# Optimization experiments

Hardware: AMD Instinct MI355X
Metric: run time of the kernel (lower is better)

Reference implementation:

```python
import jax, jax.numpy as jnp
import numpy as np

EPS = 1e-5


def _conv3x3(x, w, b):
    # x: [B,Cin,H,W], w: [Cout,Cin,3,3]
    y = jax.lax.conv_general_dilated(x, w, (1, 1), 'SAME',
                                     dimension_numbers=('NCHW', 'OIHW', 'NCHW'))
    return y + b[None, :, None, None]


def _gn_per_channel(x, w, b):
    # GroupNorm with num_groups == num_channels: per-channel spatial normalization
    mu = x.mean(axis=(2, 3), keepdims=True)
    var = x.var(axis=(2, 3), keepdims=True)
    return (x - mu) * jax.lax.rsqrt(var + EPS) * w[None, :, None, None] + b[None, :, None, None]


def _p1x1(x, w, b):
    # 1x1 conv as channel matmul. w: [Cout,Cin]
    return jnp.einsum('oc,bchw->bohw', w, x) + b[None, :, None, None]


def _cell(x, h, c, m, lc, conv_w, conv_b, gn1_w, gn1_b, convL_w, convL_b, gn2_w, gn2_b,
          wq, bq, wk, bk, wk2, bk2, wv, bv, wv2, bv2, wz, bz, wm, bm):
    # --- first conv-gate block ---
    cc = _gn_per_channel(_conv3x3(jnp.concatenate([x, h], axis=1), conv_w, conv_b), gn1_w, gn1_b)
    ci, cf, co, cg = jnp.split(cc, 4, axis=1)
    c_next = jax.nn.sigmoid(cf) * c + jax.nn.sigmoid(ci) * jnp.tanh(cg)
    # --- second (long) conv-gate block ---
    ccl = _gn_per_channel(_conv3x3(jnp.concatenate([h, c_next], axis=1), convL_w, convL_b), gn2_w, gn2_b)
    li, lf, lo, lg = jnp.split(ccl, 4, axis=1)
    lc_next = jax.nn.sigmoid(lf) * lc + jax.nn.sigmoid(li) * jnp.tanh(lg)
    c_next = jax.nn.sigmoid(lo) * jnp.tanh(lc_next)
    h_mid = jax.nn.sigmoid(co) * jnp.tanh(c_next)
    # --- SAM spatial self-attention memory ---
    B, C, H, W = h_mid.shape
    HW = H * W
    Kh = _p1x1(h_mid, wk, bk).reshape(B, -1, HW)          # [B,A,HW]
    Qh = _p1x1(h_mid, wq, bq).reshape(B, -1, HW).transpose(0, 2, 1)  # [B,HW,A]
    Vh = _p1x1(h_mid, wv, bv).reshape(B, C, HW)           # [B,C,HW]
    Km = _p1x1(m, wk2, bk2).reshape(B, -1, HW)
    Vm = _p1x1(m, wv2, bv2).reshape(B, C, HW)
    Ah = jax.nn.softmax(jnp.einsum('bpa,baq->bpq', Qh, Kh), axis=-1)  # [B,HW,HW]
    Zh = jnp.einsum('bpq,bcq->bcp', Ah, Vh).reshape(B, C, H, W)
    Am = jax.nn.softmax(jnp.einsum('bpa,baq->bpq', Qh, Km), axis=-1)
    Zm = jnp.einsum('bpq,bcq->bcp', Am, Vm).reshape(B, C, H, W)
    Z = _p1x1(jnp.concatenate([Zh, Zm], axis=1), wz, bz)  # [B,2C,H,W]
    comb = _p1x1(jnp.concatenate([Z, h_mid], axis=1), wm, bm)  # [B,3C,H,W]
    mo, mg, mi = jnp.split(comb, 3, axis=1)
    mi = jax.nn.sigmoid(mi)
    m_next = (1.0 - mi) * m + mi * jnp.tanh(mg)
    h_next = jax.nn.sigmoid(mo) * m_next
    return h_next, c_next, m_next, lc_next


def setup_inputs() -> dict:
    key = jax.random.key(0)
    B, Cin, Ch, A, H, W = 16, 64, 64, 32, 32, 32
    ks = jax.random.split(key, 24)
    s = 0.05
    inp = {
        'x': jax.random.normal(ks[0], (B, Cin, H, W), jnp.float32),
        'h': jax.random.normal(ks[1], (B, Ch, H, W), jnp.float32),
        'c': jax.random.normal(ks[2], (B, Ch, H, W), jnp.float32),
        'm': jax.random.normal(ks[3], (B, Ch, H, W), jnp.float32),
        'lc': jax.random.normal(ks[4], (B, Ch, H, W), jnp.float32),
        'conv_w': jax.random.normal(ks[5], (4 * Ch, Cin + Ch, 3, 3), jnp.float32) * s,
        'conv_b': jnp.zeros((4 * Ch,), jnp.float32),
        'gn1_w': jnp.ones((4 * Ch,), jnp.float32),
        'gn1_b': jnp.zeros((4 * Ch,), jnp.float32),
        'convL_w': jax.random.normal(ks[6], (4 * Ch, 2 * Ch, 3, 3), jnp.float32) * s,
        'convL_b': jnp.zeros((4 * Ch,), jnp.float32),
        'gn2_w': jnp.ones((4 * Ch,), jnp.float32),
        'gn2_b': jnp.zeros((4 * Ch,), jnp.float32),
        'wq': jax.random.normal(ks[7], (A, Ch), jnp.float32) * s,
        'bq': jnp.zeros((A,), jnp.float32),
        'wk': jax.random.normal(ks[8], (A, Ch), jnp.float32) * s,
        'bk': jnp.zeros((A,), jnp.float32),
        'wk2': jax.random.normal(ks[9], (A, Ch), jnp.float32) * s,
        'bk2': jnp.zeros((A,), jnp.float32),
        'wv': jax.random.normal(ks[10], (Ch, Ch), jnp.float32) * s,
        'bv': jnp.zeros((Ch,), jnp.float32),
        'wv2': jax.random.normal(ks[11], (Ch, Ch), jnp.float32) * s,
        'bv2': jnp.zeros((Ch,), jnp.float32),
        'wz': jax.random.normal(ks[12], (2 * Ch, 2 * Ch), jnp.float32) * s,
        'bz': jnp.zeros((2 * Ch,), jnp.float32),
        'wm': jax.random.normal(ks[13], (3 * Ch, 3 * Ch), jnp.float32) * s,
        'bm': jnp.zeros((3 * Ch,), jnp.float32),
    }
    return inp


def reference(x, h, c, m, lc, conv_w, conv_b, gn1_w, gn1_b, convL_w, convL_b, gn2_w, gn2_b,
              wq, bq, wk, bk, wk2, bk2, wv, bv, wv2, bv2, wz, bz, wm, bm):
    return _cell(x, h, c, m, lc, conv_w, conv_b, gn1_w, gn1_b, convL_w, convL_b, gn2_w, gn2_b,
                 wq, bq, wk, bk, wk2, bk2, wv, bv, wv2, bv2, wz, bz, wm, bm)
```

## Files before the change

kernel.cpp:

```cpp
#include <hip/hip_runtime.h>

#define DEV __device__ __forceinline__

typedef __attribute__((ext_vector_type(8))) __bf16 bf16x8;
typedef __attribute__((ext_vector_type(4))) float f32x4;
typedef __attribute__((ext_vector_type(8))) unsigned short ushort8;
typedef __attribute__((ext_vector_type(2))) unsigned short ushort2v;
typedef __attribute__((ext_vector_type(2))) unsigned int uint2v;

DEV float sigmoidf_(float x){ return 1.0f/(1.0f + __expf(-x)); }
DEV float tanhf_(float x){
    x = fminf(15.0f, fmaxf(-15.0f, x));
    float e = __expf(2.0f*x);
    return (e - 1.0f)/(e + 1.0f);
}
DEV unsigned short f2bf(float f){
    unsigned u = __builtin_bit_cast(unsigned, f);
    unsigned r = (u + 0x7FFFu + ((u>>16)&1u)) >> 16;
    return (unsigned short)r;
}
DEV float bf2f(unsigned short u){
    return __builtin_bit_cast(float, ((unsigned)u)<<16);
}
DEV unsigned cvt_pk_bf16(float lo, float hi){
    unsigned r;
    asm("v_cvt_pk_bf16_f32 %0, %1, %2" : "=v"(r) : "v"(lo), "v"(hi));
    return r;
}

__global__ __launch_bounds__(256)
void prep_kernel(const float* __restrict__ conv_w, const float* __restrict__ convL_w,
                 const float* __restrict__ wz, const float* __restrict__ wm,
                 const float* __restrict__ wq, const float* __restrict__ wk,
                 const float* __restrict__ wv, const float* __restrict__ wk2,
                 const float* __restrict__ wv2,
                 const float* __restrict__ x, const float* __restrict__ h,
                 unsigned short* __restrict__ wpk1, unsigned short* __restrict__ wpk2,
                 unsigned short* __restrict__ wzb, unsigned short* __restrict__ wmb,
                 unsigned short* __restrict__ wph, unsigned short* __restrict__ wpm,
                 unsigned short* __restrict__ buf1, unsigned short* __restrict__ buf2)
{
    __shared__ float tile[128][65];
    if (blockIdx.x < 1152) {
        int oidx = blockIdx.x*256 + threadIdx.x;
        {
            int ci5 = oidx & 31;
            int co  = (oidx >> 5) & 255;
            int kch = oidx >> 13;
            int cic = kch / 9, tap = kch - 9*cic;
            int src = co*1152 + (cic*32 + ci5)*9 + tap;
            wpk1[oidx] = f2bf(conv_w[src]);
            wpk2[oidx] = f2bf(convL_w[src]);
        }
        if (oidx < 128*128) wzb[oidx] = f2bf(wz[oidx]);
        if (oidx < 192*192) wmb[oidx] = f2bf(wm[oidx]);
        if (oidx < 32*64){
            wph[oidx]        = f2bf(wq[oidx]);
            wph[2048 + oidx] = f2bf(wk[oidx]);
            wpm[oidx]        = f2bf(wk2[oidx]);
        }
        if (oidx < 64*64){
            wph[4096 + oidx] = f2bf(wv[oidx]);
            wpm[2048 + oidx] = f2bf(wv2[oidx]);
        }
    } else if (blockIdx.x < 1184) {
        int bx2 = blockIdx.x - 1152;
        int b = bx2 >> 1;
        unsigned short* buf = (bx2 & 1) ? buf2 : buf1;
        for (int i = threadIdx.x; i < 8448; i += 256){
            int px = i >> 6, u = i & 63;
            int rr, cc2;
            if (px < 34)      { rr = 0;         cc2 = px; }
            else if (px < 68) { rr = 33;        cc2 = px-34; }
            else if (px < 100){ rr = px-68+1;   cc2 = 0; }
            else              { rr = px-100+1;  cc2 = 33; }
            reinterpret_cast<unsigned*>(buf + (size_t)(b*1156 + rr*34 + cc2)*128)[u] = 0u;
        }
    } else {
        int i  = blockIdx.x - 1184;
        int b  = (i&7)*2 + ((i>>3)&1);
        int p0 = (i>>4) * 64;
        int t  = threadIdx.x;
        for (int k=t;k<8192;k+=256){
            int ci = k>>6, pp = k&63;
            const float* s = (ci<64) ? x + (size_t)(b*64+ci)*1024
                                     : h + (size_t)(b*64+ci-64)*1024;
            tile[ci][pp] = s[p0+pp];
        }
        __syncthreads();
        for (int k=t;k<4096;k+=256){
            int pp = k>>6, c2 = k&63;
            int p  = p0 + pp;
            size_t pidx = (size_t)(b*1156 + ((p>>5)+1)*34 + (p&31) + 1);
            ushort2v v;
            v.x = f2bf(tile[c2*2][pp]);
            v.y = f2bf(tile[c2*2+1][pp]);
            *reinterpret_cast<ushort2v*>(buf1 + pidx*128 + c2*2) = v;
            if (c2 >= 32)
                *reinterpret_cast<ushort2v*>(buf2 + pidx*128 + (c2-32)*2) = v;
        }
    }
}

__global__ __launch_bounds__(256, 2)
void conv_mfma_kernel(const unsigned short* __restrict__ inp,
                      const unsigned short* __restrict__ wpk,
                      const float* __restrict__ bias,
                      unsigned short* __restrict__ out,
                      float* __restrict__ statsS, float* __restrict__ statsQ)
{
    const int bid = blockIdx.x;
    const int b   = (bid&7)*2 + ((bid>>3)&1);
    const int co0 = ((bid>>4)&3) * 64;
    const int rt  = bid>>6;
    const int r0  = rt * 4;
    const int t   = threadIdx.x;
    const int l   = t & 63;
    const int wv  = t >> 6;
    const int l15 = l & 15;
    const int lhi = l >> 4;

    __shared__ __align__(16) unsigned short in_t[26112];

    {
        const char* gsrc = reinterpret_cast<const char*>(inp + (size_t)(b*1156 + r0*34)*128);
#pragma unroll
        for (int it = 0; it < 13; ++it){
            unsigned lbase = (unsigned)(it*4096 + wv*1024);
            if (lbase < 52224u){
                unsigned beta = lbase + (unsigned)l*16u;
                unsigned soff = (beta & ~255u) + ((beta & 0xF0u) ^ (((beta>>8)&7u)<<4));
                __builtin_amdgcn_global_load_lds(
                    (const __attribute__((address_space(1))) void*)(gsrc + soff),
                    (__attribute__((address_space(3))) void*)(
                        (__attribute__((address_space(3))) char*)in_t + lbase),
                    16, 0, 0);
            }
        }
    }

    f32x4 acc[4][2];
#pragma unroll
    for (int i=0;i<4;i++)
#pragma unroll
        for (int f=0;f<2;f++)
            acc[i][f] = (f32x4){0.f,0.f,0.f,0.f};

    bf16x8 areg[4][4], breg[3][2];
#define LDA_(K, SLOT) do { const unsigned short* wrow_ = wpk + ((K)*256 + co0)*32; \
        for (int i_=0;i_<4;i_++) areg[SLOT][i_] = *reinterpret_cast<const bf16x8*>(wrow_ + (i_*16 + l15)*32 + lhi*8); } while(0)
#define LDB_(K, SLOT) do { const int cic_ = (K)/9, tap_ = (K) - 9*((K)/9); \
        const int ky_ = tap_/3, kx_ = tap_ - 3*(tap_/3); \
        for (int f_=0;f_<2;f_++){ int pl_ = (wv + ky_)*34 + (f_*16 + l15 + kx_); \
            unsigned by_ = (unsigned)(pl_*256 + cic_*64 + lhi*16) ^ (((unsigned)pl_ & 7u) << 4); \
            breg[SLOT][f_] = *reinterpret_cast<const bf16x8*>(reinterpret_cast<const char*>(in_t) + by_); } } while(0)

    LDA_(0, 0); LDA_(1, 1); LDA_(2, 2);
    __syncthreads();
    LDB_(0, 0); LDB_(1, 1);
#pragma unroll
    for (int k=0; k<36; ++k){
        const int as = k & 3, bs = k % 3;
        if (k+3 < 36) LDA_(k+3, (k+3)&3);
        if (k+2 < 36) LDB_(k+2, (k+2)%3);
        __builtin_amdgcn_s_setprio(1);
#pragma unroll
        for (int i=0;i<4;i++){
            acc[i][0] = __builtin_amdgcn_mfma_f32_16x16x32_bf16(areg[as][i], breg[bs][0], acc[i][0], 0,0,0);
            acc[i][1] = __builtin_amdgcn_mfma_f32_16x16x32_bf16(areg[as][i], breg[bs][1], acc[i][1], 0,0,0);
        }
        __builtin_amdgcn_s_setprio(0);
    }
#undef LDA_
#undef LDB_

    __syncthreads();
    float* red = reinterpret_cast<float*>(in_t);

    const int orow = r0 + wv;
    float s_ir[4][4], q_ir[4][4];
#pragma unroll
    for (int i=0;i<4;i++){
        int cobase = co0 + i*16 + lhi*4;
#pragma unroll
        for (int r=0;r<4;r++){
            float bs = bias[cobase+r];
            float e0 = acc[i][0][r] + bs;
            float e1 = acc[i][1][r] + bs;
            out[(size_t)(b*256 + cobase + r)*1024 + orow*32 + l15]      = f2bf(e0);
            out[(size_t)(b*256 + cobase + r)*1024 + orow*32 + 16 + l15] = f2bf(e1);
            s_ir[i][r] = e0 + e1;
            q_ir[i][r] = e0*e0 + e1*e1;
        }
    }
#pragma unroll
    for (int i=0;i<4;i++)
#pragma unroll
        for (int r=0;r<4;r++){
            float s = s_ir[i][r], q = q_ir[i][r];
            s += __shfl_xor(s,1); q += __shfl_xor(q,1);
            s += __shfl_xor(s,2); q += __shfl_xor(q,2);
            s += __shfl_xor(s,4); q += __shfl_xor(q,4);
            s += __shfl_xor(s,8); q += __shfl_xor(q,8);
            s_ir[i][r] = s; q_ir[i][r] = q;
        }
    if (l15 == 0){
#pragma unroll
        for (int i=0;i<4;i++)
#pragma unroll
            for (int r=0;r<4;r++){
                red[wv*64 + i*16 + lhi*4 + r]       = s_ir[i][r];
                red[256 + wv*64 + i*16 + lhi*4 + r] = q_ir[i][r];
            }
    }
    __syncthreads();
    if (t < 64){
        float S = red[t]+red[64+t]+red[128+t]+red[192+t];
        float Q = red[256+t]+red[320+t]+red[384+t]+red[448+t];
        statsS[((size_t)b*8 + rt)*256 + co0 + t] = S;
        statsQ[((size_t)b*8 + rt)*256 + co0 + t] = Q;
    }
}

__global__ __launch_bounds__(256)
void gn_gate1_kernel(const unsigned short* __restrict__ cc,
                     const float* __restrict__ statsS, const float* __restrict__ statsQ,
                     const float* __restrict__ gnw, const float* __restrict__ gnb,
                     const float* __restrict__ c_in,
                     unsigned short* __restrict__ buf2, unsigned short* __restrict__ sig_pm)
{
    const int bid = blockIdx.x;
    const int b   = (bid&7)*2 + ((bid>>3)&1);
    const int p0  = (bid>>4) * 32;
    const int t  = threadIdx.x;
    __shared__ float sc[256][2];
    __shared__ __align__(16) unsigned short cct[10240];

    {
        float S=0.f, Q=0.f;
#pragma unroll
        for (int part=0; part<8; ++part){
            S += statsS[((size_t)b*8 + part)*256 + t];
            Q += statsQ[((size_t)b*8 + part)*256 + t];
        }
        float mu  = S*(1.0f/1024.0f);
        float var = Q*(1.0f/1024.0f) - mu*mu;
        float rs  = rsqrtf(var + 1e-5f);
        float gw  = gnw[t];
        sc[t][0] = rs*gw;
        sc[t][1] = gnb[t] - mu*rs*gw;
    }
    for (int it=t; it<1024; it+=256){
        int row = it>>2, oct = it&3;
        ushort8 v = *reinterpret_cast<const ushort8*>(
            cc + (size_t)(b*256+row)*1024 + p0 + oct*8);
        *reinterpret_cast<ushort8*>(cct + row*40 + oct*8) = v;
    }
    __syncthreads();

    const int p = t & 31, cg = t >> 5;
    float cn[8], so[8];
#pragma unroll
    for (int j=0;j<8;j++){
        int ch = cg*8 + j;
        float xg[4];
#pragma unroll
        for (int g=0; g<4; g++){
            int row = g*64 + ch;
            float v = bf2f(cct[row*40 + p]);
            xg[g] = v*sc[row][0] + sc[row][1];
        }
        float cv = c_in[(size_t)(b*64+ch)*1024 + p0 + p];
        cn[j] = sigmoidf_(xg[1])*cv + sigmoidf_(xg[0])*tanhf_(xg[3]);
        so[j] = sigmoidf_(xg[2]);
    }
    ushort8 v0, s0;
#pragma unroll
    for (int j=0;j<8;j++){ v0[j]=f2bf(cn[j]); s0[j]=f2bf(so[j]); }
    int pg = p0 + p;
    size_t pidx = (size_t)(b*1156 + ((pg>>5)+1)*34 + (pg&31) + 1);
    *reinterpret_cast<ushort8*>(buf2 + pidx*128 + 64 + cg*8) = v0;
    *reinterpret_cast<ushort8*>(sig_pm + (size_t)(b*1024 + pg)*64 + cg*8) = s0;
}

__global__ __launch_bounds__(256)
void gn2_proj_kernel(const unsigned short* __restrict__ cc,
                     const float* __restrict__ statsS, const float* __restrict__ statsQ,
                     const float* __restrict__ gnw, const float* __restrict__ gnb,
                     const float* __restrict__ lc_in, const unsigned short* __restrict__ sig_pm,
                     const float* __restrict__ m_in,
                     const unsigned short* __restrict__ wph, const unsigned short* __restrict__ wpm,
                     const float* __restrict__ bq, const float* __restrict__ bk,
                     const float* __restrict__ bv, const float* __restrict__ bk2,
                     const float* __restrict__ bv2,
                     float* __restrict__ out_lc, float* __restrict__ out_c,
                     unsigned short* __restrict__ hT,
                     unsigned short* __restrict__ Qb, unsigned short* __restrict__ Khb,
                     unsigned short* __restrict__ Kmb,
                     unsigned short* __restrict__ Vhb, unsigned short* __restrict__ Vmb)
{
    const int bid = blockIdx.x;
    const int b   = (bid&7)*2 + ((bid>>3)&1);
    const int p0  = (bid>>4) * 32;
    const int t  = threadIdx.x;
    const int l  = t & 63;
    const int w  = t >> 6;
    const int l15 = l & 15, lhi = l >> 4;

    __shared__ float sc[256][2];
    __shared__ __align__(16) unsigned short cct[10240];

    {
        float S=0.f, Q=0.f;
#pragma unroll
        for (int part=0; part<8; ++part){
            S += statsS[((size_t)b*8 + part)*256 + t];
            Q += statsQ[((size_t)b*8 + part)*256 + t];
        }
        float mu  = S*(1.0f/1024.0f);
        float var = Q*(1.0f/1024.0f) - mu*mu;
        float rs  = rsqrtf(var + 1e-5f);
        float gw  = gnw[t];
        sc[t][0] = rs*gw;
        sc[t][1] = gnb[t] - mu*rs*gw;
    }
    for (int it=t; it<1024; it+=256){
        int row = it>>2, oct = it&3;
        ushort8 v = *reinterpret_cast<const ushort8*>(
            cc + (size_t)(b*256+row)*1024 + p0 + oct*8);
        *reinterpret_cast<ushort8*>(cct + row*40 + oct*8) = v;
    }
    __syncthreads();

    const int p = t & 31, cg = t >> 5;
    const size_t prow = (size_t)(b*1024 + p0 + p);
    float hm[8], mr[8];
    {
        ushort8 sv = *reinterpret_cast<const ushort8*>(sig_pm + prow*64 + cg*8);
#pragma unroll
        for (int j=0;j<8;j++){
            int ch = cg*8 + j;
            float xg[4];
#pragma unroll
            for (int g=0; g<4; g++){
                int row = g*64 + ch;
                float v = bf2f(cct[row*40 + p]);
                xg[g] = v*sc[row][0] + sc[row][1];
            }
            float lv  = lc_in[(size_t)(b*64+ch)*1024 + p0 + p];
            float lcn = sigmoidf_(xg[1])*lv + sigmoidf_(xg[0])*tanhf_(xg[3]);
            float cnx = sigmoidf_(xg[2])*tanhf_(lcn);
            out_lc[(size_t)(b*64+ch)*1024 + p0 + p] = lcn;
            out_c [(size_t)(b*64+ch)*1024 + p0 + p] = cnx;
            hm[j] = bf2f(sv[j])*tanhf_(cnx);
            mr[j] = m_in[(size_t)(b*64+ch)*1024 + p0 + p];
        }
    }
    __syncthreads();

    {
        ushort8 h0, m0;
#pragma unroll
        for (int j=0;j<8;j++){ h0[j]=f2bf(hm[j]); m0[j]=f2bf(mr[j]); }
        unsigned hb = (unsigned)(p*128) + (((unsigned)(cg*16)) ^ ((unsigned)(p&7)<<4));
        *reinterpret_cast<ushort8*>(reinterpret_cast<char*>(cct) + hb) = h0;
        *reinterpret_cast<ushort8*>(reinterpret_cast<char*>(cct) + 4096 + hb) = m0;
        *reinterpret_cast<ushort8*>(hT + prow*64 + cg*8) = h0;
    }
    __syncthreads();

    const int pass = w >> 1;
    const int pix  = (w&1)*16 + l15;
    const unsigned xsw = ((unsigned)(pix&7)) << 4;
    if (pass == 0){
        f32x4 dh[8];
#pragma unroll
        for (int i=0;i<8;i++) dh[i] = (f32x4){0.f,0.f,0.f,0.f};
#pragma unroll
        for (int ks=0; ks<2; ++ks){
            unsigned xb = (unsigned)(pix*128) + (((unsigned)(ks*64 + lhi*16)) ^ xsw);
            bf16x8 xh = *reinterpret_cast<const bf16x8*>(reinterpret_cast<const char*>(cct) + xb);
            __builtin_amdgcn_s_setprio(1);
#pragma unroll
            for (int ocf=0; ocf<8; ocf++){
                bf16x8 af = *reinterpret_cast<const bf16x8*>(
                    wph + (size_t)(ocf*16 + l15)*64 + ks*32 + lhi*8);
                dh[ocf] = __builtin_amdgcn_mfma_f32_16x16x32_bf16(af, xh, dh[ocf], 0,0,0);
            }
            __builtin_amdgcn_s_setprio(0);
        }
#pragma unroll
        for (int ocf=0; ocf<4; ocf++)
#pragma unroll
            for (int r=0;r<4;r++){
                int vc = ocf*16 + lhi*4 + r;
                Vhb[(size_t)(b*64+vc)*1024 + p0 + pix] = f2bf(dh[4+ocf][r] + bv[vc]);
            }
#pragma unroll
        for (int ocf=0; ocf<2; ocf++)
#pragma unroll
            for (int r=0;r<4;r++){
                int qc = ocf*16 + lhi*4 + r;
                unsigned byq = (unsigned)(pix*128) + (((unsigned)(qc*2))      ^ xsw);
                unsigned byk = (unsigned)(pix*128) + (((unsigned)(64 + qc*2)) ^ xsw);
                *reinterpret_cast<unsigned short*>(reinterpret_cast<char*>(cct) + 8192 + byq)
                    = f2bf(dh[ocf][r]   + bq[qc]);
                *reinterpret_cast<unsigned short*>(reinterpret_cast<char*>(cct) + 8192 + byk)
                    = f2bf(dh[2+ocf][r] + bk[qc]);
            }
    } else {
        f32x4 dm[6];
#pragma unroll
        for (int i=0;i<6;i++) dm[i] = (f32x4){0.f,0.f,0.f,0.f};
#pragma unroll
        for (int ks=0; ks<2; ++ks){
            unsigned xb = (unsigned)(pix*128) + (((unsigned)(ks*64 + lhi*16)) ^ xsw);
            bf16x8 xm = *reinterpret_cast<const bf16x8*>(
                reinterpret_cast<const char*>(cct) + 4096 + xb);
            __builtin_amdgcn_s_setprio(1);
#pragma unroll
            for (int ocf=0; ocf<6; ocf++){
                bf16x8 am = *reinterpret_cast<const bf16x8*>(
                    wpm + (size_t)(ocf*16 + l15)*64 + ks*32 + lhi*8);
                dm[ocf] = __builtin_amdgcn_mfma_f32_16x16x32_bf16(am, xm, dm[ocf], 0,0,0);
            }
            __builtin_amdgcn_s_setprio(0);
        }
#pragma unroll
        for (int ocf=0; ocf<4; ocf++)
#pragma unroll
            for (int r=0;r<4;r++){
                int vc = ocf*16 + lhi*4 + r;
                Vmb[(size_t)(b*64+vc)*1024 + p0 + pix] = f2bf(dm[2+ocf][r] + bv2[vc]);
            }
#pragma unroll
        for (int ocf=0; ocf<2; ocf++)
#pragma unroll
            for (int r=0;r<4;r++){
                int qc = ocf*16 + lhi*4 + r;
                unsigned byq = (unsigned)(pix*128) + (((unsigned)(qc*2)) ^ xsw);
                *reinterpret_cast<unsigned short*>(reinterpret_cast<char*>(cct) + 12288 + byq)
                    = f2bf(dm[ocf][r] + bk2[qc]);
            }
    }
    __syncthreads();

    {
        int pr = t>>3, oct = t&7;
        unsigned byte = (unsigned)(pr*128) + (((unsigned)(oct*16)) ^ ((unsigned)(pr&7)<<4));
        ushort8 v = *reinterpret_cast<const ushort8*>(
            reinterpret_cast<const char*>(cct) + 8192 + byte);
        if (oct < 4) *reinterpret_cast<ushort8*>(Qb  + (size_t)(b*1024+p0+pr)*32 + oct*8) = v;
        else         *reinterpret_cast<ushort8*>(Khb + (size_t)(b*1024+p0+pr)*32 + (oct-4)*8) = v;
    }
    if (t < 128){
        int pr = t>>2, oct = t&3;
        unsigned byte = (unsigned)(pr*128) + (((unsigned)(oct*16)) ^ ((unsigned)(pr&7)<<4));
        ushort8 v = *reinterpret_cast<const ushort8*>(
            reinterpret_cast<const char*>(cct) + 12288 + byte);
        *reinterpret_cast<ushort8*>(Kmb + (size_t)(b*1024+p0+pr)*32 + oct*8) = v;
    }
}

__global__ __launch_bounds__(256)
void attn_final_kernel(const unsigned short* __restrict__ Qb,
                       const unsigned short* __restrict__ Kh,
                       const unsigned short* __restrict__ Km,
                       const unsigned short* __restrict__ Vh,
                       const unsigned short* __restrict__ Vm,
                       const unsigned short* __restrict__ hT,
                       const unsigned short* __restrict__ wzb,
                       const unsigned short* __restrict__ wmb,
                       const float* __restrict__ bz, const float* __restrict__ bm,
                       const float* __restrict__ m_in,
                       float* __restrict__ out_h, float* __restrict__ out_m)
{
    const int bid  = blockIdx.x;
    const int xcd  = bid & 7;
    const int slot = bid >> 3;
    const int b    = xcd*2 + (slot>>5);
    const int p0   = (slot & 31) * 32;
    const int t   = threadIdx.x;
    const int l   = t & 63;
    const int w   = t >> 6;
    const int l15 = l & 15, g = l >> 4;
    const int pass = w >> 1;
    const int ph   = w & 1;

    __shared__ __align__(16) unsigned short Kt[2][2][2560];
    __shared__ __align__(16) unsigned short Vt[2][2][4096];
    __shared__ __align__(16) unsigned short Pt[2][2048];
    __shared__ __align__(16) unsigned short Bs[32*192];

    const bf16x8 qa = *reinterpret_cast<const bf16x8*>(
        Qb + (size_t)(b*1024 + p0 + ph*16 + l15)*32 + g*8);

    const int hrow = t>>3, hoct = t&7;
    const ushort8 hreg = *reinterpret_cast<const ushort8*>(
        hT + (size_t)(b*1024 + p0 + hrow)*64 + hoct*8);

    float m_run = -1e30f, l_run = 0.0f;
    f32x4 acc[4];
#pragma unroll
    for (int cf=0;cf<4;cf++) acc[cf] = (f32x4){0.f,0.f,0.f,0.f};

    const int krow = t>>2, koct = t&3;
    const int vrow = t>>3, voct = t&7;
    const unsigned kwb  = (unsigned)(krow*80 + koct*16);
    const unsigned vwb0 = (unsigned)(vrow*128)      + (((unsigned)voct*16) ^ ((unsigned)(vrow&7)<<4));
    const unsigned vwb1 = (unsigned)((vrow+32)*128) + (((unsigned)voct*16) ^ ((unsigned)((vrow+32)&7)<<4));

    ushort8 kr0, kr1, vv0, vv1, vv2, vv3;
#define LDSTAGE(Q0N) do { \
        kr0 = *reinterpret_cast<const ushort8*>(Kh + (size_t)(b*1024 + (Q0N) + krow)*32 + koct*8); \
        kr1 = *reinterpret_cast<const ushort8*>(Km + (size_t)(b*1024 + (Q0N) + krow)*32 + koct*8); \
        vv0 = *reinterpret_cast<const ushort8*>(Vh + (size_t)(b*64 + vrow)*1024 + (Q0N) + voct*8); \
        vv1 = *reinterpret_cast<const ushort8*>(Vh + (size_t)(b*64 + vrow+32)*1024 + (Q0N) + voct*8); \
        vv2 = *reinterpret_cast<const ushort8*>(Vm + (size_t)(b*64 + vrow)*1024 + (Q0N) + voct*8); \
        vv3 = *reinterpret_cast<const ushort8*>(Vm + (size_t)(b*64 + vrow+32)*1024 + (Q0N) + voct*8); \
    } while(0)
#define WRSTAGE(BUF) do { \
        *reinterpret_cast<ushort8*>(reinterpret_cast<char*>(Kt[0][BUF]) + kwb)  = kr0; \
        *reinterpret_cast<ushort8*>(reinterpret_cast<char*>(Kt[1][BUF]) + kwb)  = kr1; \
        *reinterpret_cast<ushort8*>(reinterpret_cast<char*>(Vt[0][BUF]) + vwb0) = vv0; \
        *reinterpret_cast<ushort8*>(reinterpret_cast<char*>(Vt[0][BUF]) + vwb1) = vv1; \
        *reinterpret_cast<ushort8*>(reinterpret_cast<char*>(Vt[1][BUF]) + vwb0) = vv2; \
        *reinterpret_cast<ushort8*>(reinterpret_cast<char*>(Vt[1][BUF]) + vwb1) = vv3; \
    } while(0)

    LDSTAGE(0);
    WRSTAGE(0);
    __syncthreads();

    const unsigned prow = (unsigned)(ph*16 + l15);
    const unsigned psw  = (prow & 7u) << 4;
    char* Pbase = reinterpret_cast<char*>(Pt[pass]);

    for (int it=0; it<16; ++it){
        const int cur = it & 1;
        if (it < 15) LDSTAGE((it+1)*64);

        f32x4 s2[4];
        __builtin_amdgcn_s_setprio(1);
#pragma unroll
        for (int qt=0; qt<4; qt++){
            const bf16x8 kb = *reinterpret_cast<const bf16x8*>(
                reinterpret_cast<const char*>(Kt[pass][cur]) + (qt*16 + l15)*80 + g*16);
            s2[qt] = __builtin_amdgcn_mfma_f32_16x16x32_bf16(kb, qa, (f32x4){0.f,0.f,0.f,0.f}, 0,0,0);
        }
        __builtin_amdgcn_s_setprio(0);

        float pm = s2[0][0];
#pragma unroll
        for (int qt=0; qt<4; qt++)
#pragma unroll
            for (int r=0;r<4;r++) pm = fmaxf(pm, s2[qt][r]);
        pm = fmaxf(pm, __shfl_xor(pm, 16));
        pm = fmaxf(pm, __shfl_xor(pm, 32));

        if (!__all(pm <= m_run + 8.0f)){
            float mn = fmaxf(m_run, pm);
            float f  = __expf(m_run - mn);
            m_run = mn;
            l_run *= f;
#pragma unroll
            for (int r=0;r<4;r++){
                float fr = __shfl(f, (l & 48) | ((l>>4)*4 + r), 64);
#pragma unroll
                for (int cf=0;cf<4;cf++) acc[cf][r] *= fr;
            }
        }

        float e[4][4];
        float lsum = 0.f;
#pragma unroll
        for (int qt=0; qt<4; qt++)
#pragma unroll
            for (int r=0;r<4;r++){
                float ev = __expf(s2[qt][r] - m_run);
                e[qt][r] = ev;
                lsum += ev;
            }
        lsum += __shfl_xor(lsum, 16);
        lsum += __shfl_xor(lsum, 32);
        l_run += lsum;

#pragma unroll
        for (int qt=0; qt<4; qt++){
            uint2v pk;
            pk.x = cvt_pk_bf16(e[qt][0], e[qt][1]);
            pk.y = cvt_pk_bf16(e[qt][2], e[qt][3]);
            unsigned byte = prow*128 + (((unsigned)(qt*32 + g*8)) ^ psw);
            *reinterpret_cast<uint2v*>(Pbase + byte) = pk;
        }

        __builtin_amdgcn_s_setprio(1);
#pragma unroll
        for (int ks=0;ks<2;ks++){
            unsigned abyte = prow*128 + (((unsigned)(ks*64 + g*16)) ^ psw);
            const bf16x8 pa = *reinterpret_cast<const bf16x8*>(Pbase + abyte);
#pragma unroll
            for (int cf=0;cf<4;cf++){
                unsigned vrw = (unsigned)(cf*16 + l15);
                unsigned vbyte = vrw*128 + (((unsigned)(ks*64 + g*16)) ^ ((vrw&7u)<<4));
                const bf16x8 vb = *reinterpret_cast<const bf16x8*>(
                    reinterpret_cast<const char*>(Vt[pass][cur]) + vbyte);
                acc[cf] = __builtin_amdgcn_mfma_f32_16x16x32_bf16(pa, vb, acc[cf], 0,0,0);
            }
        }
        __builtin_amdgcn_s_setprio(0);

        if (it < 15) WRSTAGE(cur^1);
        __syncthreads();
    }
#undef LDSTAGE
#undef WRSTAGE

    {
        float rl = 1.0f / l_run;
        float rr[4];
#pragma unroll
        for (int r=0;r<4;r++) rr[r] = __shfl(rl, (l & 48) | ((l>>4)*4 + r), 64);
#pragma unroll
        for (int cf=0;cf<4;cf++)
#pragma unroll
            for (int r=0;r<4;r++){
                unsigned pix = (unsigned)(ph*16 + g*4 + r);
                unsigned cch = (unsigned)(pass*64 + cf*16 + l15);
                unsigned byte = pix*384 + ((cch*2) ^ ((pix&7u)<<4));
                *reinterpret_cast<unsigned short*>(reinterpret_cast<char*>(Bs) + byte)
                    = f2bf(acc[cf][r]*rr[r]);
            }
    }
    {
        unsigned byte = (unsigned)(hrow*384) + 256u + (((unsigned)hoct*16) ^ ((unsigned)(hrow&7)<<4));
        *reinterpret_cast<ushort8*>(reinterpret_cast<char*>(Bs) + byte) = hreg;
    }
    __syncthreads();

    f32x4 acc1[2][2];
#pragma unroll
    for (int i=0;i<2;i++)
#pragma unroll
        for (int cf=0;cf<2;cf++) acc1[i][cf] = (f32x4){0.f,0.f,0.f,0.f};
#pragma unroll
    for (int ks=0; ks<4; ++ks){
        bf16x8 af[2];
#pragma unroll
        for (int i=0;i<2;i++)
            af[i] = *reinterpret_cast<const bf16x8*>(
                wzb + (size_t)(w*32 + i*16 + l15)*128 + ks*32 + g*8);
        __builtin_amdgcn_s_setprio(1);
#pragma unroll
        for (int cf=0;cf<2;cf++){
            unsigned p = (unsigned)(cf*16 + l15);
            unsigned byte = p*384 + (((unsigned)(ks*64 + g*16)) ^ ((p&7u)<<4));
            const bf16x8 bfr = *reinterpret_cast<const bf16x8*>(
                reinterpret_cast<const char*>(Bs) + byte);
            acc1[0][cf] = __builtin_amdgcn_mfma_f32_16x16x32_bf16(af[0], bfr, acc1[0][cf], 0,0,0);
            acc1[1][cf] = __builtin_amdgcn_mfma_f32_16x16x32_bf16(af[1], bfr, acc1[1][cf], 0,0,0);
        }
        __builtin_amdgcn_s_setprio(0);
    }
    __syncthreads();
#pragma unroll
    for (int i=0;i<2;i++){
        int co = w*32 + i*16 + g*4;
#pragma unroll
        for (int cf=0;cf<2;cf++){
            unsigned p = (unsigned)(cf*16 + l15);
#pragma unroll
            for (int r=0;r<4;r++){
                float val = acc1[i][cf][r] + bz[co+r];
                unsigned byte = p*384 + (((unsigned)((co+r)*2)) ^ ((p&7u)<<4));
                *reinterpret_cast<unsigned short*>(reinterpret_cast<char*>(Bs) + byte) = f2bf(val);
            }
        }
    }
    __syncthreads();

    f32x4 acc2[3][2];
#pragma unroll
    for (int j=0;j<3;j++)
#pragma unroll
        for (int cf=0;cf<2;cf++) acc2[j][cf] = (f32x4){0.f,0.f,0.f,0.f};
#pragma unroll
    for (int ks=0; ks<6; ++ks){
        bf16x8 am[3];
#pragma unroll
        for (int j=0;j<3;j++)
            am[j] = *reinterpret_cast<const bf16x8*>(
                wmb + (size_t)(j*64 + w*16 + l15)*192 + ks*32 + g*8);
        __builtin_amdgcn_s_setprio(1);
#pragma unroll
        for (int cf=0;cf<2;cf++){
            unsigned p = (unsigned)(cf*16 + l15);
            unsigned byte = p*384 + (((unsigned)(ks*64 + g*16)) ^ ((p&7u)<<4));
            const bf16x8 bfr = *reinterpret_cast<const bf16x8*>(
                reinterpret_cast<const char*>(Bs) + byte);
#pragma unroll
            for (int j=0;j<3;j++)
                acc2[j][cf] = __builtin_amdgcn_mfma_f32_16x16x32_bf16(am[j], bfr, acc2[j][cf], 0,0,0);
        }
        __builtin_amdgcn_s_setprio(0);
    }

    const int ch0 = w*16 + g*4;
#pragma unroll
    for (int cf=0;cf<2;cf++){
        int pix = p0 + cf*16 + l15;
#pragma unroll
        for (int r=0;r<4;r++){
            int ch = ch0 + r;
            float mo = acc2[0][cf][r] + bm[ch];
            float mg = acc2[1][cf][r] + bm[64+ch];
            float mi = sigmoidf_(acc2[2][cf][r] + bm[128+ch]);
            float mv = m_in[(size_t)(b*64+ch)*1024 + pix];
            float mn = (1.0f - mi)*mv + mi*tanhf_(mg);
            out_m[(size_t)(b*64+ch)*1024 + pix] = mn;
            out_h[(size_t)(b*64+ch)*1024 + pix] = sigmoidf_(mo)*mn;
        }
    }
}

extern "C" void kernel_launch(void* const* d_in, const int* in_sizes, int n_in,
                              void* d_out, int out_size, void* d_ws, size_t ws_size,
                              hipStream_t stream)
{
    const float* x      = (const float*)d_in[0];
    const float* h      = (const float*)d_in[1];
    const float* c      = (const float*)d_in[2];
    const float* m      = (const float*)d_in[3];
    const float* lc     = (const float*)d_in[4];
    const float* conv_w = (const float*)d_in[5];
    const float* conv_b = (const float*)d_in[6];
    const float* gn1_w  = (const float*)d_in[7];
    const float* gn1_b  = (const float*)d_in[8];
    const float* convL_w= (const float*)d_in[9];
    const float* convL_b= (const float*)d_in[10];
    const float* gn2_w  = (const float*)d_in[11];
    const float* gn2_b  = (const float*)d_in[12];
    const float* wq  = (const float*)d_in[13];
    const float* bq  = (const float*)d_in[14];
    const float* wk  = (const float*)d_in[15];
    const float* bk  = (const float*)d_in[16];
    const float* wk2 = (const float*)d_in[17];
    const float* bk2 = (const float*)d_in[18];
    const float* wv  = (const float*)d_in[19];
    const float* bv  = (const float*)d_in[20];
    const float* wv2 = (const float*)d_in[21];
    const float* bv2 = (const float*)d_in[22];
    const float* wz  = (const float*)d_in[23];
    const float* bz  = (const float*)d_in[24];
    const float* wmw = (const float*)d_in[25];
    const float* bm  = (const float*)d_in[26];

    float* out = (float*)d_out;
    float* F = (float*)d_ws;
    unsigned short* cc_bf  = (unsigned short*)F;
    unsigned short* buf1   = (unsigned short*)(F + 2097152);
    unsigned short* buf2   = (unsigned short*)(F + 3280896);
    unsigned short* hT     = (unsigned short*)(F + 4464640);
    unsigned short* Qb     = (unsigned short*)(F + 4988928);
    unsigned short* Khb    = (unsigned short*)(F + 5251072);
    unsigned short* Kmb    = (unsigned short*)(F + 5513216);
    unsigned short* Vhb    = (unsigned short*)(F + 5775360);
    unsigned short* Vmb    = (unsigned short*)(F + 6299648);
    unsigned short* sig_pm = (unsigned short*)(F + 6823936);
    unsigned short* wpk1   = (unsigned short*)(F + 7348224);
    unsigned short* wpk2   = (unsigned short*)(F + 7495680);
    unsigned short* wzb    = (unsigned short*)(F + 7643136);
    unsigned short* wmb    = (unsigned short*)(F + 7651328);
    unsigned short* wph    = (unsigned short*)(F + 7669760);
    unsigned short* wpm    = (unsigned short*)(F + 7673856);
    float*          statsS = F + 7676928;
    float*          statsQ = F + 7709696;

    dim3 blk256(256);
    prep_kernel<<<dim3(1440), blk256, 0, stream>>>(conv_w, convL_w, wz, wmw,
                                                   wq, wk, wv, wk2, wv2, x, h,
                                                   wpk1, wpk2, wzb, wmb, wph, wpm,
                                                   buf1, buf2);
    conv_mfma_kernel<<<dim3(512), blk256, 0, stream>>>(buf1, wpk1, conv_b, cc_bf, statsS, statsQ);
    gn_gate1_kernel<<<dim3(512), blk256, 0, stream>>>(cc_bf, statsS, statsQ, gn1_w, gn1_b, c,
                                                      buf2, sig_pm);
    conv_mfma_kernel<<<dim3(512), blk256, 0, stream>>>(buf2, wpk2, convL_b, cc_bf, statsS, statsQ);
    gn2_proj_kernel<<<dim3(512), blk256, 0, stream>>>(cc_bf, statsS, statsQ, gn2_w, gn2_b,
                                                      lc, sig_pm, m, wph, wpm,
                                                      bq, bk, bv, bk2, bv2,
                                                      out + 3*1048576 ,
                                                      out + 1*1048576 ,
                                                      hT, Qb, Khb, Kmb, Vhb, Vmb);
    attn_final_kernel<<<dim3(512), blk256, 0, stream>>>(Qb, Khb, Kmb, Vhb, Vmb, hT,
                                                        wzb, wmb, bz, bm, m,
                                                        out , out + 2*1048576 );
    (void)in_sizes; (void)n_in; (void)out_size; (void)ws_size;
}
```

Before: 104.0 us.

## Widen attention block to 64 queries and deepen conv weight prefetch

The attention/final kernel now runs 512-thread blocks covering 64 query pixels, using half as many blocks. Each K/V tile staged in shared memory is therefore reused by twice as many queries, which cuts global K/V traffic per query. The wz and wm projection epilogues are re-split across the eight waves. Separately, the conv MFMA kernel prefetches A-weight fragments five steps ahead instead of three, hiding more load latency at the cost of extra registers. That register growth, plus the larger LDS footprint and fewer blocks, may lower occupancy.

```diff
diff --git a/kernel.cpp b/kernel.cpp
--- a/kernel.cpp
+++ b/kernel.cpp
@@ -146,7 +146,7 @@
         for (int f=0;f<2;f++)
             acc[i][f] = (f32x4){0.f,0.f,0.f,0.f};
 
-    bf16x8 areg[4][4], breg[3][2];
+    bf16x8 areg[6][4], breg[3][2];
 #define LDA_(K, SLOT) do { const unsigned short* wrow_ = wpk + ((K)*256 + co0)*32; \
         for (int i_=0;i_<4;i_++) areg[SLOT][i_] = *reinterpret_cast<const bf16x8*>(wrow_ + (i_*16 + l15)*32 + lhi*8); } while(0)
 #define LDB_(K, SLOT) do { const int cic_ = (K)/9, tap_ = (K) - 9*((K)/9); \
@@ -155,13 +155,13 @@
             unsigned by_ = (unsigned)(pl_*256 + cic_*64 + lhi*16) ^ (((unsigned)pl_ & 7u) << 4); \
             breg[SLOT][f_] = *reinterpret_cast<const bf16x8*>(reinterpret_cast<const char*>(in_t) + by_); } } while(0)
 
-    LDA_(0, 0); LDA_(1, 1); LDA_(2, 2);
+    LDA_(0, 0); LDA_(1, 1); LDA_(2, 2); LDA_(3, 3); LDA_(4, 4);
     __syncthreads();
     LDB_(0, 0); LDB_(1, 1);
 #pragma unroll
     for (int k=0; k<36; ++k){
-        const int as = k & 3, bs = k % 3;
-        if (k+3 < 36) LDA_(k+3, (k+3)&3);
+        const int as = k % 6, bs = k % 3;
+        if (k+5 < 36) LDA_(k+5, (k+5)%6);
         if (k+2 < 36) LDB_(k+2, (k+2)%3);
         __builtin_amdgcn_s_setprio(1);
 #pragma unroll
@@ -462,7 +462,7 @@
     }
 }
 
-__global__ __launch_bounds__(256)
+__global__ __launch_bounds__(512)
 void attn_final_kernel(const unsigned short* __restrict__ Qb,
                        const unsigned short* __restrict__ Kh,
                        const unsigned short* __restrict__ Km,
@@ -476,24 +476,22 @@
                        float* __restrict__ out_h, float* __restrict__ out_m)
 {
     const int bid  = blockIdx.x;
-    const int xcd  = bid & 7;
-    const int slot = bid >> 3;
-    const int b    = xcd*2 + (slot>>5);
-    const int p0   = (slot & 31) * 32;
+    const int b    = (bid&7)*2 + ((bid>>3)&1);
+    const int p0   = (bid>>4) * 64;
     const int t   = threadIdx.x;
     const int l   = t & 63;
     const int w   = t >> 6;
     const int l15 = l & 15, g = l >> 4;
-    const int pass = w >> 1;
-    const int ph   = w & 1;
+    const int pass = w >> 2;
+    const int wq   = w & 3;
 
     __shared__ __align__(16) unsigned short Kt[2][2][2560];
     __shared__ __align__(16) unsigned short Vt[2][2][4096];
-    __shared__ __align__(16) unsigned short Pt[2][2048];
-    __shared__ __align__(16) unsigned short Bs[32*192];
+    __shared__ __align__(16) unsigned short Pt[2][4096];
+    __shared__ __align__(16) unsigned short Bs[64*192];
 
     const bf16x8 qa = *reinterpret_cast<const bf16x8*>(
-        Qb + (size_t)(b*1024 + p0 + ph*16 + l15)*32 + g*8);
+        Qb + (size_t)(b*1024 + p0 + wq*16 + l15)*32 + g*8);
 
     const int hrow = t>>3, hoct = t&7;
     const ushort8 hreg = *reinterpret_cast<const ushort8*>(
@@ -504,35 +502,30 @@
 #pragma unroll
     for (int cf=0;cf<4;cf++) acc[cf] = (f32x4){0.f,0.f,0.f,0.f};
 
-    const int krow = t>>2, koct = t&3;
-    const int vrow = t>>3, voct = t&7;
-    const unsigned kwb  = (unsigned)(krow*80 + koct*16);
-    const unsigned vwb0 = (unsigned)(vrow*128)      + (((unsigned)voct*16) ^ ((unsigned)(vrow&7)<<4));
-    const unsigned vwb1 = (unsigned)((vrow+32)*128) + (((unsigned)voct*16) ^ ((unsigned)((vrow+32)&7)<<4));
-
-    ushort8 kr0, kr1, vv0, vv1, vv2, vv3;
+    const int ktens = t>>8;
+    const int krow  = (t>>2)&63, koct = t&3;
+    const int vrow  = t>>3, voct = t&7;
+    const unsigned kwb = (unsigned)(krow*80 + koct*16);
+    const unsigned vwb = (unsigned)(vrow*128) + (((unsigned)voct*16) ^ ((unsigned)(vrow&7)<<4));
+    const unsigned short* Kgsrc = ktens ? Km : Kh;
+
+    ushort8 kr0, vv0, vv1;
 #define LDSTAGE(Q0N) do { \
-        kr0 = *reinterpret_cast<const ushort8*>(Kh + (size_t)(b*1024 + (Q0N) + krow)*32 + koct*8); \
-        kr1 = *reinterpret_cast<const ushort8*>(Km + (size_t)(b*1024 + (Q0N) + krow)*32 + koct*8); \
+        kr0 = *reinterpret_cast<const ushort8*>(Kgsrc + (size_t)(b*1024 + (Q0N) + krow)*32 + koct*8); \
         vv0 = *reinterpret_cast<const ushort8*>(Vh + (size_t)(b*64 + vrow)*1024 + (Q0N) + voct*8); \
-        vv1 = *reinterpret_cast<const ushort8*>(Vh + (size_t)(b*64 + vrow+32)*1024 + (Q0N) + voct*8); \
-        vv2 = *reinterpret_cast<const ushort8*>(Vm + (size_t)(b*64 + vrow)*1024 + (Q0N) + voct*8); \
-        vv3 = *reinterpret_cast<const ushort8*>(Vm + (size_t)(b*64 + vrow+32)*1024 + (Q0N) + voct*8); \
+        vv1 = *reinterpret_cast<const ushort8*>(Vm + (size_t)(b*64 + vrow)*1024 + (Q0N) + voct*8); \
     } while(0)
 #define WRSTAGE(BUF) do { \
-        *reinterpret_cast<ushort8*>(reinterpret_cast<char*>(Kt[0][BUF]) + kwb)  = kr0; \
-        *reinterpret_cast<ushort8*>(reinterpret_cast<char*>(Kt[1][BUF]) + kwb)  = kr1; \
-        *reinterpret_cast<ushort8*>(reinterpret_cast<char*>(Vt[0][BUF]) + vwb0) = vv0; \
-        *reinterpret_cast<ushort8*>(reinterpret_cast<char*>(Vt[0][BUF]) + vwb1) = vv1; \
-        *reinterpret_cast<ushort8*>(reinterpret_cast<char*>(Vt[1][BUF]) + vwb0) = vv2; \
-        *reinterpret_cast<ushort8*>(reinterpret_cast<char*>(Vt[1][BUF]) + vwb1) = vv3; \
+        *reinterpret_cast<ushort8*>(reinterpret_cast<char*>(Kt[ktens][BUF]) + kwb) = kr0; \
+        *reinterpret_cast<ushort8*>(reinterpret_cast<char*>(Vt[0][BUF]) + vwb) = vv0; \
+        *reinterpret_cast<ushort8*>(reinterpret_cast<char*>(Vt[1][BUF]) + vwb) = vv1; \
     } while(0)
 
     LDSTAGE(0);
     WRSTAGE(0);
     __syncthreads();
 
-    const unsigned prow = (unsigned)(ph*16 + l15);
+    const unsigned prow = (unsigned)(wq*16 + l15);
     const unsigned psw  = (prow & 7u) << 4;
     char* Pbase = reinterpret_cast<char*>(Pt[pass]);
 
@@ -625,7 +618,7 @@
         for (int cf=0;cf<4;cf++)
 #pragma unroll
             for (int r=0;r<4;r++){
-                unsigned pix = (unsigned)(ph*16 + g*4 + r);
+                unsigned pix = (unsigned)(wq*16 + g*4 + r);
                 unsigned cch = (unsigned)(pass*64 + cf*16 + l15);
                 unsigned byte = pix*384 + ((cch*2) ^ ((pix&7u)<<4));
                 *reinterpret_cast<unsigned short*>(reinterpret_cast<char*>(Bs) + byte)
@@ -638,6 +631,7 @@
     }
     __syncthreads();
 
+    const int wk4 = w & 3, ph2 = w >> 2;
     f32x4 acc1[2][2];
 #pragma unroll
     for (int i=0;i<2;i++)
@@ -649,11 +643,11 @@
 #pragma unroll
         for (int i=0;i<2;i++)
             af[i] = *reinterpret_cast<const bf16x8*>(
-                wzb + (size_t)(w*32 + i*16 + l15)*128 + ks*32 + g*8);
+                wzb + (size_t)(wk4*32 + i*16 + l15)*128 + ks*32 + g*8);
         __builtin_amdgcn_s_setprio(1);
 #pragma unroll
         for (int cf=0;cf<2;cf++){
-            unsigned p = (unsigned)(cf*16 + l15);
+            unsigned p = (unsigned)(ph2*32 + cf*16 + l15);
             unsigned byte = p*384 + (((unsigned)(ks*64 + g*16)) ^ ((p&7u)<<4));
             const bf16x8 bfr = *reinterpret_cast<const bf16x8*>(
                 reinterpret_cast<const char*>(Bs) + byte);
@@ -665,10 +659,10 @@
     __syncthreads();
 #pragma unroll
     for (int i=0;i<2;i++){
-        int co = w*32 + i*16 + g*4;
+        int co = wk4*32 + i*16 + g*4;
 #pragma unroll
         for (int cf=0;cf<2;cf++){
-            unsigned p = (unsigned)(cf*16 + l15);
+            unsigned p = (unsigned)(ph2*32 + cf*16 + l15);
 #pragma unroll
             for (int r=0;r<4;r++){
                 float val = acc1[i][cf][r] + bz[co+r];
@@ -690,11 +684,11 @@
 #pragma unroll
         for (int j=0;j<3;j++)
             am[j] = *reinterpret_cast<const bf16x8*>(
-                wmb + (size_t)(j*64 + w*16 + l15)*192 + ks*32 + g*8);
+                wmb + (size_t)(j*64 + wk4*16 + l15)*192 + ks*32 + g*8);
         __builtin_amdgcn_s_setprio(1);
 #pragma unroll
         for (int cf=0;cf<2;cf++){
-            unsigned p = (unsigned)(cf*16 + l15);
+            unsigned p = (unsigned)(ph2*32 + cf*16 + l15);
             unsigned byte = p*384 + (((unsigned)(ks*64 + g*16)) ^ ((p&7u)<<4));
             const bf16x8 bfr = *reinterpret_cast<const bf16x8*>(
                 reinterpret_cast<const char*>(Bs) + byte);
@@ -705,10 +699,10 @@
         __builtin_amdgcn_s_setprio(0);
     }
 
-    const int ch0 = w*16 + g*4;
+    const int ch0 = wk4*16 + g*4;
 #pragma unroll
     for (int cf=0;cf<2;cf++){
-        int pix = p0 + cf*16 + l15;
+        int pix = p0 + ph2*32 + cf*16 + l15;
 #pragma unroll
         for (int r=0;r<4;r++){
             int ch = ch0 + r;
@@ -791,8 +785,8 @@
                                                       out + 3*1048576 ,
                                                       out + 1*1048576 ,
                                                       hT, Qb, Khb, Kmb, Vhb, Vmb);
-    attn_final_kernel<<<dim3(512), blk256, 0, stream>>>(Qb, Khb, Kmb, Vhb, Vmb, hT,
-                                                        wzb, wmb, bz, bm, m,
-                                                        out , out + 2*1048576 );
+    attn_final_kernel<<<dim3(256), dim3(512), 0, stream>>>(Qb, Khb, Kmb, Vhb, Vmb, hT,
+                                                           wzb, wmb, bz, bm, m,
+                                                           out , out + 2*1048576 );
     (void)in_sizes; (void)n_in; (void)out_size; (void)ws_size;
 }
```

Result: no change. 103.6 us (median of 2 runs) (-0.4%).
